# Kernel tuning notes

Hardware: AMD Instinct MI355X
Metric: run time of the kernel (lower is better)

The kernel has to match this reference:

```python
import jax, jax.numpy as jnp
import numpy as np
import math

NUM_HEADS = 8
C_RATIO = 0.5

def _dwconv(x, w, b, pad):
    # x: [B,C,H,W], w: [C,1,kh,kw] depthwise
    y = jax.lax.conv_general_dilated(x, w, (1, 1), [(pad, pad), (pad, pad)],
                                     dimension_numbers=('NCHW', 'OIHW', 'NCHW'),
                                     feature_group_count=x.shape[1])
    return y + b[None, :, None, None]

def setup_inputs():
    key = jax.random.key(0)
    ks = jax.random.split(key, 16)
    B, H, W, C = 2, 128, 128, 384
    cr = int(C * C_RATIO)  # 192
    cg = C // 3            # 128
    s = 0.02
    return {
        'x': jax.random.normal(ks[0], (B, H * W, C), jnp.float32),
        'red_w1': jax.random.normal(ks[1], (cg, 1, 1, 1), jnp.float32) * s,
        'red_b1': jnp.zeros((cg,), jnp.float32),
        'red_w3': jax.random.normal(ks[2], (cg, 1, 3, 3), jnp.float32) * s,
        'red_b3': jnp.zeros((cg,), jnp.float32),
        'red_w5': jax.random.normal(ks[3], (cg, 1, 5, 5), jnp.float32) * s,
        'red_b5': jnp.zeros((cg,), jnp.float32),
        'fus_w': jax.random.normal(ks[4], (cr, C, 4, 4), jnp.float32) * s,
        'fus_b': jnp.zeros((cr,), jnp.float32),
        'q_w': jax.random.normal(ks[5], (C, cr), jnp.float32) * s,
        'k_w': jax.random.normal(ks[6], (cr, cr), jnp.float32) * s,
        'v_w': jax.random.normal(ks[7], (cr, C), jnp.float32) * s,
        'cpe_w': jax.random.normal(ks[8], (C, 1, 3, 3), jnp.float32) * s,
        'cpe_b': jnp.zeros((C,), jnp.float32),
        'proj_w': jax.random.normal(ks[9], (C, C), jnp.float32) * s,
        'proj_b': jnp.zeros((C,), jnp.float32),
        'H': 128,
        'W': 128,
    }

def reference(x, red_w1, red_b1, red_w3, red_b3, red_w5, red_b5,
              fus_w, fus_b, q_w, k_w, v_w, cpe_w, cpe_b, proj_w, proj_b, H, W):
    B, N, C = x.shape
    cr = q_w.shape[1]
    hd = C // NUM_HEADS
    dk = cr // NUM_HEADS
    scale = (hd * C_RATIO) ** -0.5
    _time = max(int(math.log(H // 16, 4)), int(math.log(W // 16, 4)))
    _scale = 4 ** _time  # == 4 for our shapes

    _x = x.transpose(0, 2, 1).reshape(B, C, H, W)
    x1, x2, x3 = jnp.split(_x, 3, axis=1)
    y1 = _dwconv(x1, red_w1, red_b1, 0)                       # applied once
    y2 = _dwconv(_dwconv(x2, red_w3, red_b3, 1), red_w3, red_b3, 1)  # twice
    y3 = x3
    for _ in range(3):                                        # thrice
        y3 = _dwconv(y3, red_w5, red_b5, 2)
    fused = jnp.concatenate([y1, y2, y3], axis=1)             # [B,C,H,W]

    f = jax.lax.conv_general_dilated(fused, fus_w, (4, 4), [(0, 0), (0, 0)],
                                     dimension_numbers=('NCHW', 'OIHW', 'NCHW'))
    f = jax.nn.gelu(f + fus_b[None, :, None, None], approximate=False)
    _xr = f.reshape(B, cr, -1).transpose(0, 2, 1)             # [B, L, cr], L = (H/4)*(W/4)

    q = (x @ q_w).reshape(B, N, NUM_HEADS, dk).transpose(0, 2, 1, 3)    # [B,h,N,dk]
    k = (_xr @ k_w).reshape(B, -1, NUM_HEADS, dk).transpose(0, 2, 1, 3) # [B,h,L,dk]
    v = (_xr @ v_w).reshape(B, -1, NUM_HEADS, hd).transpose(0, 2, 1, 3) # [B,h,L,hd]

    attn = jax.nn.softmax(jnp.einsum('bhnd,bhld->bhnl', q, k) * scale, axis=-1)

    Hs, Ws = H // _scale, W // _scale
    v_sp = v.transpose(0, 2, 1, 3).reshape(B, -1, C).transpose(0, 2, 1).reshape(B, C, Hs, Ws)
    v = v + _dwconv(v_sp, cpe_w, cpe_b, 1).reshape(B, C, -1).reshape(
        B, NUM_HEADS, hd, -1).transpose(0, 1, 3, 2)

    out = jnp.einsum('bhnl,bhld->bhnd', attn, v).transpose(0, 2, 1, 3).reshape(B, N, C)
    return out @ proj_w + proj_b
```

## Files before the change

kernel.cpp:

```cpp
#include <hip/hip_runtime.h>
#include <math.h>

typedef short short8 __attribute__((ext_vector_type(8)));
typedef float f32x4 __attribute__((ext_vector_type(4)));

#define B_    2
#define HH    128
#define WW    128
#define NPIX  16384
#define C_    384
#define CR    192
#define CG    128
#define NH    8
#define DK    24
#define HD    48
#define LL    1024
#define KFUS  6144
#define SCALE_L2E 0.29448889f

__device__ __forceinline__ float bf2f(short h) {
    union { unsigned u; float f; } v; v.u = ((unsigned)(unsigned short)h) << 16; return v.f;
}
__device__ __forceinline__ short f2bf(float f) {
    union { float f; unsigned u; } v; v.f = f;
    unsigned r = v.u + 0x7fffu + ((v.u >> 16) & 1u);
    return (short)(unsigned short)(r >> 16);
}
__device__ __forceinline__ short f2bf_fast(float f) {
    union { float f; unsigned u; } v; v.f = f;
    return (short)(unsigned short)((v.u + 0x8000u) >> 16);
}
__device__ __forceinline__ float exp2b(float x) {
#if __has_builtin(__builtin_amdgcn_exp2f)
    return __builtin_amdgcn_exp2f(x);
#else
    return exp2f(x);
#endif
}
__device__ __forceinline__ unsigned cvt_pk_bf16(float lo, float hi) {
    unsigned r;
    asm("v_cvt_pk_bf16_f32 %0, %1, %2" : "=v"(r) : "v"(lo), "v"(hi));
    return r;
}

template<int PATCH, int KS, int STRIDE>
__global__ __launch_bounds__(256) void dwconv_k(
    const float* __restrict__ in, int in_off,
    float* __restrict__ outf, short* __restrict__ outp, int out_coff,
    const float* __restrict__ w, const float* __restrict__ bias)
{
    constexpr int pad = KS / 2;
    constexpr int NV = 4 + KS - 1;
    int idx = blockIdx.x * 256 + threadIdx.x;
    int c    = idx & (CG - 1);
    int pix4 = (idx >> 7) & 4095;
    int b    = idx >> 19;
    int y = pix4 >> 5, x0 = (pix4 & 31) << 2;
    float wl[KS * KS];
    #pragma unroll
    for (int i = 0; i < KS * KS; i++) wl[i] = w[c * KS * KS + i];
    float bv = bias[c];
    float acc[4] = {bv, bv, bv, bv};
    #pragma unroll
    for (int ky = 0; ky < KS; ky++) {
        int yy = y + ky - pad;
        if ((unsigned)yy >= HH) continue;
        const float* rowp = &in[(size_t)(b * NPIX + yy * WW) * STRIDE + in_off + c];
        float v[NV];
        #pragma unroll
        for (int j = 0; j < NV; j++) {
            int xx = x0 + j - pad;
            v[j] = ((unsigned)xx < WW) ? rowp[(size_t)xx * STRIDE] : 0.f;
        }
        #pragma unroll
        for (int kx = 0; kx < KS; kx++)
            #pragma unroll
            for (int o = 0; o < 4; o++)
                acc[o] += v[o + kx] * wl[ky * KS + kx];
    }
    if (!PATCH) {
        float* op = &outf[(size_t)(b * NPIX + y * WW + x0) * CG + c];
        #pragma unroll
        for (int o = 0; o < 4; o++) op[(size_t)o * CG] = acc[o];
    } else {
        int m = b * LL + (y >> 2) * 32 + (x0 >> 2);
        short* op = &outp[(size_t)m * KFUS + ((y & 3) * 4) * C_ + out_coff + c];
        #pragma unroll
        for (int o = 0; o < 4; o++) op[(size_t)o * C_] = f2bf(acc[o]);
    }
}

__global__ __launch_bounds__(256) void prep_k(
    const float* __restrict__ fus_w, const float* __restrict__ k_w,
    const float* __restrict__ v_w, const float* __restrict__ q_w,
    const float* __restrict__ proj_w,
    short* __restrict__ Wt, short* __restrict__ Bkv,
    short* __restrict__ qw_b, short* __restrict__ pw_b)
{
    int idx = blockIdx.x * 256 + threadIdx.x;
    const int NW = KFUS * CR;
    if (idx < NW) {
        int k = idx / CR, oc = idx - k * CR;
        int p = k / C_,  ic = k - p * C_;
        Wt[idx] = f2bf(fus_w[(oc * C_ + ic) * 16 + p]);
        return;
    }
    idx -= NW;
    if (idx < CR * 576) {
        int k = idx / 576, n = idx - k * 576;
        Bkv[idx] = f2bf((n < CR) ? k_w[k * CR + n] : v_w[k * C_ + (n - CR)]);
        return;
    }
    idx -= CR * 576;
    if (idx < C_ * CR) { qw_b[idx] = f2bf(q_w[idx]); return; }
    idx -= C_ * CR;
    if (idx < C_ * C_) pw_b[idx] = f2bf(proj_w[idx]);
}

template<int AF, int CF>
__global__ __launch_bounds__(256) void gemm_k(
    const void* __restrict__ Av, const short* __restrict__ Bm, void* __restrict__ Cv,
    const float* __restrict__ bias, int M, int N, int K)
{
    __shared__ short a_lds[64 * 40];
    __shared__ short bT_lds[64 * 40];
    int tid = threadIdx.x;
    int lane = tid & 63, wave = tid >> 6, quad = lane >> 4, l16 = lane & 15;
    int bm = blockIdx.x * 64, bn = blockIdx.y * 64;
    int wm = (wave >> 1) * 32, wn = (wave & 1) * 32;
    f32x4 z4 = {0.f, 0.f, 0.f, 0.f};
    f32x4 acc00 = z4, acc01 = z4, acc10 = z4, acc11 = z4;
    int arow = tid >> 2, aseg = tid & 3;
    int bk = tid >> 3, bnseg = tid & 7;

    for (int k0 = 0; k0 < K; k0 += 32) {
        __syncthreads();
        if (AF) {
            const float* Af = (const float*)Av;
            const float4* p = (const float4*)&Af[(size_t)(bm + arow) * K + k0 + aseg * 8];
            float4 f0 = p[0], f1 = p[1];
            short8 av;
            av[0] = f2bf_fast(f0.x); av[1] = f2bf_fast(f0.y);
            av[2] = f2bf_fast(f0.z); av[3] = f2bf_fast(f0.w);
            av[4] = f2bf_fast(f1.x); av[5] = f2bf_fast(f1.y);
            av[6] = f2bf_fast(f1.z); av[7] = f2bf_fast(f1.w);
            *(short8*)&a_lds[arow * 40 + aseg * 8] = av;
        } else {
            const short* Ab = (const short*)Av;
            *(short8*)&a_lds[arow * 40 + aseg * 8] =
                *(const short8*)&Ab[(size_t)(bm + arow) * K + k0 + aseg * 8];
        }
        short8 bv = *(const short8*)&Bm[(size_t)(k0 + bk) * N + bn + bnseg * 8];
        #pragma unroll
        for (int i = 0; i < 8; i++) bT_lds[(bnseg * 8 + i) * 40 + bk] = bv[i];
        __syncthreads();
        short8 a0 = *(short8*)&a_lds[(wm + l16) * 40 + quad * 8];
        short8 a1 = *(short8*)&a_lds[(wm + 16 + l16) * 40 + quad * 8];
        short8 b0 = *(short8*)&bT_lds[(wn + l16) * 40 + quad * 8];
        short8 b1 = *(short8*)&bT_lds[(wn + 16 + l16) * 40 + quad * 8];
        acc00 = __builtin_amdgcn_mfma_f32_16x16x32_bf16(a0, b0, acc00, 0, 0, 0);
        acc01 = __builtin_amdgcn_mfma_f32_16x16x32_bf16(a0, b1, acc01, 0, 0, 0);
        acc10 = __builtin_amdgcn_mfma_f32_16x16x32_bf16(a1, b0, acc10, 0, 0, 0);
        acc11 = __builtin_amdgcn_mfma_f32_16x16x32_bf16(a1, b1, acc11, 0, 0, 0);
    }
    f32x4 accs[2][2] = {{acc00, acc01}, {acc10, acc11}};
    #pragma unroll
    for (int mt = 0; mt < 2; mt++)
      #pragma unroll
      for (int nt = 0; nt < 2; nt++) {
        int col = bn + wn + nt * 16 + l16;
        float bvv = bias ? bias[col] : 0.f;
        #pragma unroll
        for (int r = 0; r < 4; r++) {
            int row = bm + wm + mt * 16 + quad * 4 + r;
            float v = accs[mt][nt][r] + bvv;
            if (CF) ((float*)Cv)[(size_t)row * N + col] = v;
            else    ((short*)Cv)[(size_t)row * N + col] = f2bf(v);
        }
      }
}

__global__ __launch_bounds__(256) void gemm_part_k(
    const short* __restrict__ A, const short* __restrict__ Bm,
    float* __restrict__ Cpart, int M, int N, int K, int kchunk)
{
    __shared__ short a_lds[64 * 40];
    __shared__ short bT_lds[64 * 40];
    int tid = threadIdx.x;
    int lane = tid & 63, wave = tid >> 6, quad = lane >> 4, l16 = lane & 15;
    int bm = blockIdx.x * 64, bn = blockIdx.y * 64;
    int kbeg = blockIdx.z * kchunk, kend = kbeg + kchunk;
    int wm = (wave >> 1) * 32, wn = (wave & 1) * 32;
    f32x4 z4 = {0.f, 0.f, 0.f, 0.f};
    f32x4 acc00 = z4, acc01 = z4, acc10 = z4, acc11 = z4;
    int arow = tid >> 2, aseg = tid & 3;
    int bk = tid >> 3, bnseg = tid & 7;

    for (int k0 = kbeg; k0 < kend; k0 += 32) {
        __syncthreads();
        *(short8*)&a_lds[arow * 40 + aseg * 8] =
            *(const short8*)&A[(size_t)(bm + arow) * K + k0 + aseg * 8];
        short8 bv = *(const short8*)&Bm[(size_t)(k0 + bk) * N + bn + bnseg * 8];
        #pragma unroll
        for (int i = 0; i < 8; i++) bT_lds[(bnseg * 8 + i) * 40 + bk] = bv[i];
        __syncthreads();
        short8 a0 = *(short8*)&a_lds[(wm + l16) * 40 + quad * 8];
        short8 a1 = *(short8*)&a_lds[(wm + 16 + l16) * 40 + quad * 8];
        short8 b0 = *(short8*)&bT_lds[(wn + l16) * 40 + quad * 8];
        short8 b1 = *(short8*)&bT_lds[(wn + 16 + l16) * 40 + quad * 8];
        acc00 = __builtin_amdgcn_mfma_f32_16x16x32_bf16(a0, b0, acc00, 0, 0, 0);
        acc01 = __builtin_amdgcn_mfma_f32_16x16x32_bf16(a0, b1, acc01, 0, 0, 0);
        acc10 = __builtin_amdgcn_mfma_f32_16x16x32_bf16(a1, b0, acc10, 0, 0, 0);
        acc11 = __builtin_amdgcn_mfma_f32_16x16x32_bf16(a1, b1, acc11, 0, 0, 0);
    }
    float* Cs = Cpart + (size_t)blockIdx.z * M * N;
    f32x4 accs[2][2] = {{acc00, acc01}, {acc10, acc11}};
    #pragma unroll
    for (int mt = 0; mt < 2; mt++)
      #pragma unroll
      for (int nt = 0; nt < 2; nt++) {
        int col = bn + wn + nt * 16 + l16;
        #pragma unroll
        for (int r = 0; r < 4; r++) {
            int row = bm + wm + mt * 16 + quad * 4 + r;
            Cs[(size_t)row * N + col] = accs[mt][nt][r];
        }
      }
}

__global__ __launch_bounds__(256) void fusred_k(
    const float* __restrict__ part, const float* __restrict__ bias,
    short* __restrict__ xr)
{
    const int MN = 2048 * CR;
    int idx = blockIdx.x * 256 + threadIdx.x;
    float v = part[idx] + part[idx + MN] + part[idx + 2 * MN] + part[idx + 3 * MN]
            + bias[idx % CR];
    v = 0.5f * v * (1.f + erff(v * 0.70710678118f));
    xr[idx] = f2bf(v);
}

__global__ __launch_bounds__(256) void cpe_k(
    const short* __restrict__ kv, const float* __restrict__ cw,
    const float* __restrict__ cb, short* __restrict__ v2)
{
    int idx = blockIdx.x * 256 + threadIdx.x;
    int c = idx % C_;
    int t = idx / C_;
    int l = t & (LL - 1);
    int b = t >> 10;
    int y = l >> 5, x = l & 31;
    const short* vp = kv + CR;
    float acc = bf2f(vp[(size_t)(b * LL + l) * 576 + c]) + cb[c];
    #pragma unroll
    for (int ky = 0; ky < 3; ky++) {
        int yy = y + ky - 1; if ((unsigned)yy >= 32) continue;
        #pragma unroll
        for (int kx = 0; kx < 3; kx++) {
            int xx = x + kx - 1; if ((unsigned)xx >= 32) continue;
            acc += bf2f(vp[(size_t)(b * LL + yy * 32 + xx) * 576 + c])
                 * cw[c * 9 + ky * 3 + kx];
        }
    }
    v2[(size_t)(b * LL + l) * C_ + c] = f2bf(acc);
}

__global__ __launch_bounds__(256) void transp_k(
    const short* __restrict__ v2b, const short* __restrict__ kvb,
    short* __restrict__ v2t, short* __restrict__ kpack)
{
    int tid = threadIdx.x;
    if (blockIdx.x < 256) {
        __shared__ short t_lds[64 * 49];
        int bh = blockIdx.x >> 4, b = bh >> 3, h = bh & 7;
        int l0 = (blockIdx.x & 15) << 6;
        for (int i = tid; i < 64 * 48; i += 256) {
            int dl = i / 48, f = i - dl * 48;
            t_lds[dl * 49 + f] = v2b[(size_t)(b * LL + l0 + dl) * C_ + h * HD + f];
        }
        __syncthreads();
        for (int i = tid; i < 64 * 48; i += 256) {
            int f = i >> 6, dl = i & 63;
            v2t[((size_t)bh * 48 + f) * LL + l0 + dl] = t_lds[dl * 49 + f];
        }
    } else {
        int gid = (blockIdx.x - 256) * 256 + tid;
        int j = gid & 31, t = gid >> 5;
        int l = t & (LL - 1), bh = t >> 10;
        int b = bh >> 3, h = bh & 7;
        kpack[gid] = (j < 24) ? kvb[(size_t)(b * LL + l) * 576 + h * DK + j] : (short)0;
    }
}

__global__ __launch_bounds__(256, 4) void attn_k(
    const short* __restrict__ qbuf, const short* __restrict__ kpack,
    const short* __restrict__ v2t, short* __restrict__ obuf)
{
    int tid = threadIdx.x;
    int lane = tid & 63, wave = tid >> 6, quad = lane >> 4, l16 = lane & 15;
    int bh = blockIdx.y, b = bh >> 3, h = bh & 7;
    int q0 = blockIdx.x * 256 + wave * 64;

    short8 qf[4];
    #pragma unroll
    for (int qt = 0; qt < 4; qt++) {
        short8 z = {0, 0, 0, 0, 0, 0, 0, 0};
        qf[qt] = z;
        if (quad < 3) {
            short8 raw = *(const short8*)&qbuf[(size_t)(b * NPIX + q0 + qt * 16 + l16) * CR + h * DK + quad * 8];
            #pragma unroll
            for (int i = 0; i < 8; i++) qf[qt][i] = f2bf(bf2f(raw[i]) * SCALE_L2E);
        }
    }

    f32x4 z4 = {0.f, 0.f, 0.f, 0.f};
    f32x4 oacc[4][3] = {{z4, z4, z4}, {z4, z4, z4}, {z4, z4, z4}, {z4, z4, z4}};
    float rs[4] = {0.f, 0.f, 0.f, 0.f};

    int krow = ((l16 >> 2) << 3) + (l16 & 3);
    const short* kp1 = kpack + (((size_t)bh) << 15) + krow * 32 + quad * 8;
    const short* vp0 = v2t + ((size_t)bh * 48 + l16) * LL + quad * 8;
    const short* vp1 = vp0 + 16 * LL;
    const short* vp2 = vp0 + 32 * LL;

    short8 kf1 = *(const short8*)&kp1[0];
    short8 kf2 = *(const short8*)&kp1[128];

    for (int kt = 0; kt < 32; kt++) {
        short8 av0 = *(const short8*)&vp0[kt << 5];
        short8 av1 = *(const short8*)&vp1[kt << 5];
        short8 av2 = *(const short8*)&vp2[kt << 5];
        int ktn = (kt + 1) & 31;
        short8 nkf1 = *(const short8*)&kp1[ktn << 10];
        short8 nkf2 = *(const short8*)&kp1[(ktn << 10) + 128];
        #pragma unroll
        for (int qt = 0; qt < 4; qt++) {
            f32x4 s1 = __builtin_amdgcn_mfma_f32_16x16x32_bf16(kf1, qf[qt], z4, 0, 0, 0);
            f32x4 s2 = __builtin_amdgcn_mfma_f32_16x16x32_bf16(kf2, qf[qt], z4, 0, 0, 0);
            float e0 = exp2b(s1[0]), e1 = exp2b(s1[1]);
            float e2 = exp2b(s1[2]), e3 = exp2b(s1[3]);
            float g0 = exp2b(s2[0]), g1 = exp2b(s2[1]);
            float g2 = exp2b(s2[2]), g3 = exp2b(s2[3]);
            rs[qt] += ((e0 + e1) + (e2 + e3)) + ((g0 + g1) + (g2 + g3));
            union { unsigned u[4]; short8 s; } pb;
            pb.u[0] = cvt_pk_bf16(e0, e1);
            pb.u[1] = cvt_pk_bf16(e2, e3);
            pb.u[2] = cvt_pk_bf16(g0, g1);
            pb.u[3] = cvt_pk_bf16(g2, g3);
            oacc[qt][0] = __builtin_amdgcn_mfma_f32_16x16x32_bf16(av0, pb.s, oacc[qt][0], 0, 0, 0);
            oacc[qt][1] = __builtin_amdgcn_mfma_f32_16x16x32_bf16(av1, pb.s, oacc[qt][1], 0, 0, 0);
            oacc[qt][2] = __builtin_amdgcn_mfma_f32_16x16x32_bf16(av2, pb.s, oacc[qt][2], 0, 0, 0);
        }
        kf1 = nkf1; kf2 = nkf2;
    }

    #pragma unroll
    for (int qt = 0; qt < 4; qt++) {
        float s = rs[qt];
        s += __shfl_xor(s, 16);
        s += __shfl_xor(s, 32);
        float inv = 1.0f / s;
        short* orow = &obuf[(size_t)(b * NPIX + q0 + qt * 16 + l16) * C_ + h * HD + quad * 4];
        #pragma unroll
        for (int nt = 0; nt < 3; nt++) {
            uint2 ov;
            ov.x = cvt_pk_bf16(oacc[qt][nt][0] * inv, oacc[qt][nt][1] * inv);
            ov.y = cvt_pk_bf16(oacc[qt][nt][2] * inv, oacc[qt][nt][3] * inv);
            *(uint2*)&orow[nt * 16] = ov;
        }
    }
}

extern "C" void kernel_launch(void* const* d_in, const int* in_sizes, int n_in,
                              void* d_out, int out_size, void* d_ws, size_t ws_size,
                              hipStream_t stream)
{
    const float* x      = (const float*)d_in[0];
    const float* red_w1 = (const float*)d_in[1];
    const float* red_b1 = (const float*)d_in[2];
    const float* red_w3 = (const float*)d_in[3];
    const float* red_b3 = (const float*)d_in[4];
    const float* red_w5 = (const float*)d_in[5];
    const float* red_b5 = (const float*)d_in[6];
    const float* fus_w  = (const float*)d_in[7];
    const float* fus_b  = (const float*)d_in[8];
    const float* q_w    = (const float*)d_in[9];
    const float* k_w    = (const float*)d_in[10];
    const float* v_w    = (const float*)d_in[11];
    const float* cpe_w  = (const float*)d_in[12];
    const float* cpe_b  = (const float*)d_in[13];
    const float* proj_w = (const float*)d_in[14];
    const float* proj_b = (const float*)d_in[15];
    float* out = (float*)d_out;

    char* ws = (char*)d_ws;
    short* A_fus = (short*)(ws +         0);
    short* obuf  = A_fus;
    float* tmpA  = (float*)(ws +  25165824);
    short* qbuf  = (short*)(ws +  25165824);
    float* tmpB  = (float*)(ws +  41943040);
    float* part  = (float*)(ws +  41943040);
    short* v2t   = (short*)(ws +  48234496);
    short* kpack = (short*)(ws +  49807360);
    short* Wt    = (short*)(ws +  58720256);
    short* Bkv   = (short*)(ws +  61079552);
    short* qw_b  = (short*)(ws +  61300736);
    short* pw_b  = (short*)(ws +  61448192);
    short* xr    = (short*)(ws +  61743104);
    short* kvb   = (short*)(ws +  62529536);
    short* v2b   = (short*)(ws +  64888832);
    (void)in_sizes; (void)n_in; (void)out_size; (void)ws_size;

    dim3 blk(256);
    dwconv_k<1,1,C_><<<dim3(4096), blk, 0, stream>>>(x,    0,   nullptr, A_fus, 0,   red_w1, red_b1);
    dwconv_k<0,3,C_><<<dim3(4096), blk, 0, stream>>>(x,    128, tmpA,  nullptr, 0,   red_w3, red_b3);
    dwconv_k<1,3,CG><<<dim3(4096), blk, 0, stream>>>(tmpA, 0,   nullptr, A_fus, 128, red_w3, red_b3);
    dwconv_k<0,5,C_><<<dim3(4096), blk, 0, stream>>>(x,    256, tmpB,  nullptr, 0,   red_w5, red_b5);
    dwconv_k<0,5,CG><<<dim3(4096), blk, 0, stream>>>(tmpB, 0,   tmpA,  nullptr, 0,   red_w5, red_b5);
    dwconv_k<1,5,CG><<<dim3(4096), blk, 0, stream>>>(tmpA, 0,   nullptr, A_fus, 256, red_w5, red_b5);
    prep_k<<<dim3(5904), blk, 0, stream>>>(fus_w, k_w, v_w, q_w, proj_w, Wt, Bkv, qw_b, pw_b);
    gemm_part_k<<<dim3(32, 3, 4), blk, 0, stream>>>(A_fus, Wt, part, 2048, CR, KFUS, KFUS / 4);
    fusred_k<<<dim3(1536), blk, 0, stream>>>(part, fus_b, xr);
    gemm_k<0,0><<<dim3(32, 9), blk, 0, stream>>>(xr, Bkv, kvb, (const float*)nullptr, 2048, 576, CR);
    cpe_k<<<dim3(3072), blk, 0, stream>>>(kvb, cpe_w, cpe_b, v2b);
    transp_k<<<dim3(2304), blk, 0, stream>>>(v2b, kvb, v2t, kpack);
    gemm_k<1,0><<<dim3(512, 3), blk, 0, stream>>>(x, qw_b, qbuf, (const float*)nullptr, 32768, CR, C_);
    attn_k<<<dim3(64, 16), blk, 0, stream>>>(qbuf, kpack, v2t, obuf);
    gemm_k<0,1><<<dim3(512, 6), blk, 0, stream>>>(obuf, pw_b, out, proj_b, 32768, C_, C_);
}
```

Measured before the change: 398.2 us.

## Tile K and V^T into contiguous MFMA blocks and prefetch V fragments

```diff
diff --git a/kernel.cpp b/kernel.cpp
--- a/kernel.cpp
+++ b/kernel.cpp
@@ -281,14 +281,20 @@
         __syncthreads();
         for (int i = tid; i < 64 * 48; i += 256) {
             int f = i >> 6, dl = i & 63;
-            v2t[((size_t)bh * 48 + f) * LL + l0 + dl] = t_lds[dl * 49 + f];
+            int l = l0 + dl;
+            v2t[(size_t)bh * 49152 + (size_t)((l >> 5) * 3 + (f >> 4)) * 512
+                + (f & 15) * 32 + (l & 31)] = t_lds[dl * 49 + f];
         }
     } else {
         int gid = (blockIdx.x - 256) * 256 + tid;
         int j = gid & 31, t = gid >> 5;
         int l = t & (LL - 1), bh = t >> 10;
         int b = bh >> 3, h = bh & 7;
-        kpack[gid] = (j < 24) ? kvb[(size_t)(b * LL + l) * 576 + h * DK + j] : (short)0;
+        int jj = l & 31, a = jj >> 3, c = jj & 7;
+        int s = (c < 4) ? (a * 4 + c) : (16 + a * 4 + (c - 4));
+        int lp = (l & ~31) | s;
+        kpack[(size_t)bh * 32768 + lp * 32 + j] =
+            (j < 24) ? kvb[(size_t)(b * LL + l) * 576 + h * DK + j] : (short)0;
     }
 }
 
@@ -317,22 +323,22 @@
     f32x4 oacc[4][3] = {{z4, z4, z4}, {z4, z4, z4}, {z4, z4, z4}, {z4, z4, z4}};
     float rs[4] = {0.f, 0.f, 0.f, 0.f};
 
-    int krow = ((l16 >> 2) << 3) + (l16 & 3);
-    const short* kp1 = kpack + (((size_t)bh) << 15) + krow * 32 + quad * 8;
-    const short* vp0 = v2t + ((size_t)bh * 48 + l16) * LL + quad * 8;
-    const short* vp1 = vp0 + 16 * LL;
-    const short* vp2 = vp0 + 32 * LL;
-
-    short8 kf1 = *(const short8*)&kp1[0];
-    short8 kf2 = *(const short8*)&kp1[128];
+    const short* kp = kpack + (((size_t)bh) << 15) + l16 * 32 + quad * 8;
+    const short* vt = v2t + (size_t)bh * 49152 + l16 * 32 + quad * 8;
+
+    short8 kf1 = *(const short8*)&kp[0];
+    short8 kf2 = *(const short8*)&kp[512];
+    short8 av0 = *(const short8*)&vt[0];
+    short8 av1 = *(const short8*)&vt[512];
+    short8 av2 = *(const short8*)&vt[1024];
 
     for (int kt = 0; kt < 32; kt++) {
-        short8 av0 = *(const short8*)&vp0[kt << 5];
-        short8 av1 = *(const short8*)&vp1[kt << 5];
-        short8 av2 = *(const short8*)&vp2[kt << 5];
         int ktn = (kt + 1) & 31;
-        short8 nkf1 = *(const short8*)&kp1[ktn << 10];
-        short8 nkf2 = *(const short8*)&kp1[(ktn << 10) + 128];
+        short8 nk1 = *(const short8*)&kp[ktn << 10];
+        short8 nk2 = *(const short8*)&kp[(ktn << 10) + 512];
+        short8 nv0 = *(const short8*)&vt[(ktn * 3) << 9];
+        short8 nv1 = *(const short8*)&vt[((ktn * 3 + 1)) << 9];
+        short8 nv2 = *(const short8*)&vt[((ktn * 3 + 2)) << 9];
         #pragma unroll
         for (int qt = 0; qt < 4; qt++) {
             f32x4 s1 = __builtin_amdgcn_mfma_f32_16x16x32_bf16(kf1, qf[qt], z4, 0, 0, 0);
@@ -351,7 +357,7 @@
             oacc[qt][1] = __builtin_amdgcn_mfma_f32_16x16x32_bf16(av1, pb.s, oacc[qt][1], 0, 0, 0);
             oacc[qt][2] = __builtin_amdgcn_mfma_f32_16x16x32_bf16(av2, pb.s, oacc[qt][2], 0, 0, 0);
         }
-        kf1 = nkf1; kf2 = nkf2;
+        kf1 = nk1; kf2 = nk2; av0 = nv0; av1 = nv1; av2 = nv2;
     }
 
     #pragma unroll
```

Result: no change. 392.1 us (-1.6%).
